# Optimization experiments

Hardware: AMD Instinct MI355X
Metric: run time of the kernel (lower is better)

Reference implementation:

```python
import jax, jax.numpy as jnp
import numpy as np

N_NODES = 50000
N_EDGES = 500000
H_DIM = 128
OUT_DIM = 16
N_RELS = 90
N_BASES = 4


def setup_inputs() -> dict:
    key = jax.random.key(0)
    ks = jax.random.split(key, 12)
    inp = {
        'node_ids': jnp.arange(N_NODES, dtype=jnp.int32),
        'src': jax.random.randint(ks[0], (N_EDGES,), 0, N_NODES, dtype=jnp.int32),
        'dst': jax.random.randint(ks[1], (N_EDGES,), 0, N_NODES, dtype=jnp.int32),
        'etype': jax.random.randint(ks[2], (N_EDGES,), 0, N_RELS, dtype=jnp.int32),
        'emb': jax.random.normal(ks[3], (N_NODES, H_DIM), jnp.float32),
        'basis1': jax.random.normal(ks[4], (N_BASES, H_DIM, H_DIM), jnp.float32) * (1.0 / np.sqrt(H_DIM)),
        'comp1': jax.random.normal(ks[5], (N_RELS, N_BASES), jnp.float32) * (1.0 / np.sqrt(N_BASES)),
        'loop_w1': jax.random.normal(ks[6], (H_DIM, H_DIM), jnp.float32) * (1.0 / np.sqrt(H_DIM)),
        'bias1': jnp.zeros((H_DIM,), jnp.float32),
        'basis2': jax.random.normal(ks[7], (N_BASES, H_DIM, OUT_DIM), jnp.float32) * (1.0 / np.sqrt(H_DIM)),
        'comp2': jax.random.normal(ks[8], (N_RELS, N_BASES), jnp.float32) * (1.0 / np.sqrt(N_BASES)),
        'loop_w2': jax.random.normal(ks[9], (H_DIM, OUT_DIM), jnp.float32) * (1.0 / np.sqrt(H_DIM)),
        'bias2': jnp.zeros((OUT_DIM,), jnp.float32),
    }
    return inp


def _rel_graph_conv(x, src, dst, etype, basis, comp, loop_w, bias, num_nodes):
    # Basis decomposition: W_r = sum_b comp[r,b] * basis[b].
    # Project node features through each basis first (N is smaller than E),
    # then combine per-edge with relation coefficients: avoids per-edge GEMM.
    xb = jnp.einsum('ni,bio->nbo', x, basis)            # [N, B, out]
    msg = jnp.einsum('eb,ebo->eo', comp[etype], xb[src])  # [E, out]
    agg = jax.ops.segment_sum(msg, dst, num_segments=num_nodes)  # [N, out]
    # apply_norm=True: divide aggregated messages by in-degree of dst.
    deg = jax.ops.segment_sum(jnp.ones((src.shape[0],), x.dtype), dst,
                              num_segments=num_nodes)
    h = agg * (1.0 / jnp.maximum(deg, 1.0))[:, None]
    # self_loop=True plus bias.
    return h + x @ loop_w + bias


def reference(node_ids, src, dst, etype, emb, basis1, comp1, loop_w1, bias1,
              basis2, comp2, loop_w2, bias2):
    n = emb.shape[0]
    x = emb[node_ids]                                   # embedding lookup
    h = jax.nn.relu(_rel_graph_conv(x, src, dst, etype, basis1, comp1,
                                    loop_w1, bias1, n))
    out = _rel_graph_conv(h, src, dst, etype, basis2, comp2, loop_w2, bias2, n)
    return out
```

## Files before the change

kernel.cpp:

```cpp
#include <hip/hip_runtime.h>
#include <hip/hip_bf16.h>

#define N_NODES 50000
#define N_EDGES 500000
#define H_DIM 128
#define OUT_DIM 16
#define KDIM 640

typedef short short8 __attribute__((ext_vector_type(8)));
typedef float f32x4 __attribute__((ext_vector_type(4)));
typedef float f32x2 __attribute__((ext_vector_type(2)));

__device__ inline unsigned short f2b(float f) {
  unsigned u = __float_as_uint(f);
  u += 0x7fffu + ((u >> 16) & 1u);
  return (unsigned short)(u >> 16);
}
__device__ inline float b2f(unsigned short u) {
  return __uint_as_float(((unsigned)u) << 16);
}

#define CONV_BLOCKS 6250
#define PREP_BLOCKS 360
#define INIT_BLOCKS 196
__global__ void prologue_kernel(const int* __restrict__ node_ids, const float* __restrict__ emb,
                                unsigned short* __restrict__ Abuf,
                                const float* __restrict__ basis1, const float* __restrict__ loop_w1,
                                const float* __restrict__ basis2, const float* __restrict__ loop_w2,
                                unsigned short* __restrict__ B1t, unsigned short* __restrict__ B2pt,
                                int* __restrict__ cntA, int* __restrict__ cntB,
                                int* __restrict__ counter) {
  int b = blockIdx.x;
  if (b < CONV_BLOCKS) {
    int tid = b * 256 + threadIdx.x;
    if (tid >= N_NODES * (H_DIM / 4)) return;
    int n = tid >> 5;
    int q = tid & 31;
    int id = node_ids[n];
    const float4 v = *reinterpret_cast<const float4*>(emb + (size_t)id * H_DIM + q * 4);
    uint2 p;
    p.x = (unsigned)f2b(v.x) | ((unsigned)f2b(v.y) << 16);
    p.y = (unsigned)f2b(v.z) | ((unsigned)f2b(v.w) << 16);
    *reinterpret_cast<uint2*>(Abuf + (size_t)n * KDIM + 512 + q * 4) = p;
  } else if (b < CONV_BLOCKS + PREP_BLOCKS) {
    int tid = (b - CONV_BLOCKS) * 256 + threadIdx.x;
    if (tid < 128 * KDIM) {
      int c = tid / KDIM, k = tid % KDIM;
      float v = (k < 512) ? basis1[k * 128 + c] : loop_w1[(k - 512) * 128 + c];
      B1t[c * KDIM + k] = f2b(v);
    } else if (tid < 128 * KDIM + 80 * 128) {
      int t2 = tid - 128 * KDIM;
      int c = t2 / 128, k = t2 % 128;
      float v = (c < 64) ? basis2[(c >> 4) * 128 * 16 + k * 16 + (c & 15)]
                         : loop_w2[k * 16 + (c - 64)];
      B2pt[c * 128 + k] = f2b(v);
    }
  } else {
    int i = (b - CONV_BLOCKS - PREP_BLOCKS) * 256 + threadIdx.x;
    if (i < N_NODES) {
      cntA[i] = 0;
      cntB[i] = 0;
    }
    if (i == 0) *counter = 0;
  }
}

__global__ void count_kernel(const int* __restrict__ dst, int* __restrict__ cnt) {
  for (int e = blockIdx.x * blockDim.x + threadIdx.x; e < N_EDGES; e += gridDim.x * blockDim.x)
    atomicAdd(&cnt[dst[e]], 1);
}

__global__ void alloc_kernel(const int* __restrict__ cnt, int* __restrict__ start,
                             int* __restrict__ counter) {
  int i = blockIdx.x * blockDim.x + threadIdx.x;
  int lane = threadIdx.x & 63;
  int c = (i < N_NODES) ? cnt[i] : 0;
  int incl = c;
#pragma unroll
  for (int off = 1; off < 64; off <<= 1) {
    int v = __shfl_up(incl, off, 64);
    if (lane >= off) incl += v;
  }
  int waveTotal = __shfl(incl, 63, 64);
  int base = 0;
  if (lane == 63) base = atomicAdd(counter, waveTotal);
  base = __shfl(base, 63, 64);
  if (i < N_NODES) start[i] = base + incl - c;
}

__global__ void fill_kernel(const int* __restrict__ src, const int* __restrict__ dst,
                            const int* __restrict__ et, const int* __restrict__ csr_start,
                            int* __restrict__ cnt, int2* __restrict__ csr_se) {
  for (int e = blockIdx.x * blockDim.x + threadIdx.x; e < N_EDGES; e += gridDim.x * blockDim.x) {
    int d = dst[e];
    int idx = csr_start[d] + atomicAdd(&cnt[d], 1);
    csr_se[idx] = make_int2(src[e], et[e]);
  }
}

__global__ __launch_bounds__(256) void agg_kernel(const int* __restrict__ csr_start,
                                                  const int* __restrict__ csr_cnt,
                                                  const int2* __restrict__ csr_se,
                                                  const float* __restrict__ comp,
                                                  unsigned short* __restrict__ Abuf) {
  int node = blockIdx.x * 4 + (threadIdx.x >> 6);
  if (node >= N_NODES) return;
  int lane = threadIdx.x & 63;
  int lo = __builtin_amdgcn_readfirstlane(csr_start[node]);
  int deg = __builtin_amdgcn_readfirstlane(csr_cnt[node]);
  int hi = lo + deg;

  f32x2 a0 = {0.f, 0.f}, a1 = {0.f, 0.f}, a2 = {0.f, 0.f}, a3 = {0.f, 0.f};
  const unsigned short* featb = Abuf + 512;
  const int laneoff = lane * 2;

#define EDGE_BODY(S, T)                                                              \
  {                                                                                  \
    unsigned u = *reinterpret_cast<const unsigned*>(featb + (size_t)(S)*KDIM + laneoff); \
    float4 c = *reinterpret_cast<const float4*>(comp + (T)*4);                       \
    f32x2 x;                                                                         \
    x.x = __uint_as_float(u << 16);                                                  \
    x.y = __uint_as_float(u & 0xffff0000u);                                          \
    a0 = __builtin_elementwise_fma((f32x2){c.x, c.x}, x, a0);                        \
    a1 = __builtin_elementwise_fma((f32x2){c.y, c.y}, x, a1);                        \
    a2 = __builtin_elementwise_fma((f32x2){c.z, c.z}, x, a2);                        \
    a3 = __builtin_elementwise_fma((f32x2){c.w, c.w}, x, a3);                        \
  }

  int e = lo;
  for (; e + 4 <= hi; e += 4) {
    int2 p0 = csr_se[e], p1 = csr_se[e + 1], p2 = csr_se[e + 2], p3 = csr_se[e + 3];
    int s0 = __builtin_amdgcn_readfirstlane(p0.x), t0 = __builtin_amdgcn_readfirstlane(p0.y);
    int s1 = __builtin_amdgcn_readfirstlane(p1.x), t1 = __builtin_amdgcn_readfirstlane(p1.y);
    int s2 = __builtin_amdgcn_readfirstlane(p2.x), t2 = __builtin_amdgcn_readfirstlane(p2.y);
    int s3 = __builtin_amdgcn_readfirstlane(p3.x), t3 = __builtin_amdgcn_readfirstlane(p3.y);
    EDGE_BODY(s0, t0)
    EDGE_BODY(s1, t1)
    EDGE_BODY(s2, t2)
    EDGE_BODY(s3, t3)
  }
  for (; e < hi; ++e) {
    int2 p = csr_se[e];
    int s0 = __builtin_amdgcn_readfirstlane(p.x), t0 = __builtin_amdgcn_readfirstlane(p.y);
    EDGE_BODY(s0, t0)
  }
#undef EDGE_BODY

  float inv = 1.0f / (float)(deg > 0 ? deg : 1);
  unsigned short* out = Abuf + (size_t)node * KDIM;
  unsigned p0w = (unsigned)f2b(a0.x * inv) | ((unsigned)f2b(a0.y * inv) << 16);
  unsigned p1w = (unsigned)f2b(a1.x * inv) | ((unsigned)f2b(a1.y * inv) << 16);
  unsigned p2w = (unsigned)f2b(a2.x * inv) | ((unsigned)f2b(a2.y * inv) << 16);
  unsigned p3w = (unsigned)f2b(a3.x * inv) | ((unsigned)f2b(a3.y * inv) << 16);
  *reinterpret_cast<unsigned*>(out + 0 * 128 + laneoff) = p0w;
  *reinterpret_cast<unsigned*>(out + 1 * 128 + laneoff) = p1w;
  *reinterpret_cast<unsigned*>(out + 2 * 128 + laneoff) = p2w;
  *reinterpret_cast<unsigned*>(out + 3 * 128 + laneoff) = p3w;
}

__global__ __launch_bounds__(256) void agg2_kernel(const int* __restrict__ csr_start,
                                                   const int* __restrict__ csr_cnt,
                                                   const int2* __restrict__ csr_se,
                                                   const float* __restrict__ comp,
                                                   const unsigned short* __restrict__ Abuf,
                                                   const float* __restrict__ bias2,
                                                   float* __restrict__ dout) {
  int node = blockIdx.x * 4 + (threadIdx.x >> 6);
  if (node >= N_NODES) return;
  int lane = threadIdx.x & 63;
  int bsel = lane >> 4;
  int o = lane & 15;
  int lo = __builtin_amdgcn_readfirstlane(csr_start[node]);
  int deg = __builtin_amdgcn_readfirstlane(csr_cnt[node]);
  int hi = lo + deg;

  float acc = 0.f;

#define EDGE2_BODY(S, T)                                                   \
  {                                                                        \
    unsigned short u = Abuf[(size_t)(S)*KDIM + lane];                      \
    float4 c = *reinterpret_cast<const float4*>(comp + (T)*4);             \
    float cb = (bsel < 2) ? ((bsel == 0) ? c.x : c.y)                      \
                          : ((bsel == 2) ? c.z : c.w);                     \
    acc = fmaf(cb, b2f(u), acc);                                           \
  }

  int e = lo;
  for (; e + 4 <= hi; e += 4) {
    int2 p0 = csr_se[e], p1 = csr_se[e + 1], p2 = csr_se[e + 2], p3 = csr_se[e + 3];
    int s0 = __builtin_amdgcn_readfirstlane(p0.x), t0 = __builtin_amdgcn_readfirstlane(p0.y);
    int s1 = __builtin_amdgcn_readfirstlane(p1.x), t1 = __builtin_amdgcn_readfirstlane(p1.y);
    int s2 = __builtin_amdgcn_readfirstlane(p2.x), t2 = __builtin_amdgcn_readfirstlane(p2.y);
    int s3 = __builtin_amdgcn_readfirstlane(p3.x), t3 = __builtin_amdgcn_readfirstlane(p3.y);
    EDGE2_BODY(s0, t0)
    EDGE2_BODY(s1, t1)
    EDGE2_BODY(s2, t2)
    EDGE2_BODY(s3, t3)
  }
  for (; e < hi; ++e) {
    int2 p = csr_se[e];
    int s0 = __builtin_amdgcn_readfirstlane(p.x), t0 = __builtin_amdgcn_readfirstlane(p.y);
    EDGE2_BODY(s0, t0)
  }
#undef EDGE2_BODY

  acc += __shfl_xor(acc, 16, 64);
  acc += __shfl_xor(acc, 32, 64);

  if (lane < 16) {
    float inv = 1.0f / (float)(deg > 0 ? deg : 1);
    float sl = b2f(Abuf[(size_t)node * KDIM + 64 + o]);
    dout[(size_t)node * OUT_DIM + o] = acc * inv + sl + bias2[o];
  }
}

template <int NC, int KT, bool RELU, bool HAS_BIAS>
__global__ __launch_bounds__(256) void gemm_kernel(const unsigned short* __restrict__ A,
                                                   int a_stride,
                                                   const unsigned short* __restrict__ Bt,
                                                   int bt_stride,
                                                   const float* __restrict__ bias,
                                                   unsigned short* __restrict__ outp,
                                                   int out_stride, int M) {
  __shared__ unsigned short As[64][64];
  __shared__ unsigned short Bs[NC][64];
  int wave = threadIdx.x >> 6;
  int lane = threadIdx.x & 63;
  int row0 = blockIdx.x * 64;
  f32x4 acc[NC / 16];
#pragma unroll
  for (int i = 0; i < NC / 16; ++i) acc[i] = (f32x4){0.f, 0.f, 0.f, 0.f};

  int ar = wave * 16 + (lane & 15);
  int kh = lane >> 4;

  for (int k0 = 0; k0 < KT; k0 += 64) {
#pragma unroll
    for (int p = 0; p < 2; ++p) {
      int cid = threadIdx.x + p * 256;
      int r = cid >> 3, c8 = cid & 7;
      int gr = row0 + r;
      short8 v = {};
      if (gr < M) v = *reinterpret_cast<const short8*>(A + (size_t)gr * a_stride + k0 + c8 * 8);
      *reinterpret_cast<short8*>(&As[r][(c8 ^ (r & 7)) * 8]) = v;
    }
    for (int cid = threadIdx.x; cid < NC * 8; cid += 256) {
      int r = cid >> 3, c8 = cid & 7;
      short8 v = *reinterpret_cast<const short8*>(Bt + (size_t)r * bt_stride + k0 + c8 * 8);
      *reinterpret_cast<short8*>(&Bs[r][(c8 ^ (r & 7)) * 8]) = v;
    }
    __syncthreads();
    short8 a0 = *reinterpret_cast<const short8*>(&As[ar][((kh) ^ (ar & 7)) * 8]);
    short8 a1 = *reinterpret_cast<const short8*>(&As[ar][((4 + kh) ^ (ar & 7)) * 8]);
#pragma unroll
    for (int ct = 0; ct < NC / 16; ++ct) {
      int bc = ct * 16 + (lane & 15);
      short8 b0 = *reinterpret_cast<const short8*>(&Bs[bc][((kh) ^ (bc & 7)) * 8]);
      short8 b1 = *reinterpret_cast<const short8*>(&Bs[bc][((4 + kh) ^ (bc & 7)) * 8]);
      acc[ct] = __builtin_amdgcn_mfma_f32_16x16x32_bf16(a0, b0, acc[ct], 0, 0, 0);
      acc[ct] = __builtin_amdgcn_mfma_f32_16x16x32_bf16(a1, b1, acc[ct], 0, 0, 0);
    }
    __syncthreads();
  }
  int col_l = lane & 15;
  int rb = row0 + wave * 16 + (lane >> 4) * 4;
#pragma unroll
  for (int ct = 0; ct < NC / 16; ++ct) {
    int col = ct * 16 + col_l;
    float bv = HAS_BIAS ? bias[col] : 0.f;
#pragma unroll
    for (int r = 0; r < 4; ++r) {
      int gr = rb + r;
      if (gr < M) {
        float v = acc[ct][r] + bv;
        if (RELU) v = fmaxf(v, 0.0f);
        outp[(size_t)gr * out_stride + col] = f2b(v);
      }
    }
  }
}

extern "C" void kernel_launch(void* const* d_in, const int* in_sizes, int n_in,
                              void* d_out, int out_size, void* d_ws, size_t ws_size,
                              hipStream_t stream) {
  const int* node_ids = (const int*)d_in[0];
  const int* src = (const int*)d_in[1];
  const int* dst = (const int*)d_in[2];
  const int* etype = (const int*)d_in[3];
  const float* emb = (const float*)d_in[4];
  const float* basis1 = (const float*)d_in[5];
  const float* comp1 = (const float*)d_in[6];
  const float* loop_w1 = (const float*)d_in[7];
  const float* bias1 = (const float*)d_in[8];
  const float* basis2 = (const float*)d_in[9];
  const float* comp2 = (const float*)d_in[10];
  const float* loop_w2 = (const float*)d_in[11];
  const float* bias2 = (const float*)d_in[12];
  (void)in_sizes; (void)n_in; (void)out_size; (void)ws_size;

  char* ws = (char*)d_ws;
  size_t off = 0;
  auto alloc = [&](size_t bytes) -> void* {
    void* p = ws + off;
    off += (bytes + 255) & ~(size_t)255;
    return p;
  };
  int* csr_start = (int*)alloc(N_NODES * sizeof(int));
  int* cntA = (int*)alloc(N_NODES * sizeof(int));
  int* cntB = (int*)alloc(N_NODES * sizeof(int));
  int* counter = (int*)alloc(sizeof(int));
  int2* csr_se = (int2*)alloc((size_t)N_EDGES * sizeof(int2));
  unsigned short* Abuf = (unsigned short*)alloc((size_t)N_NODES * KDIM * sizeof(unsigned short));
  unsigned short* B1t = (unsigned short*)alloc(128 * KDIM * sizeof(unsigned short));
  unsigned short* B2pt = (unsigned short*)alloc(80 * 128 * sizeof(unsigned short));

  prologue_kernel<<<CONV_BLOCKS + PREP_BLOCKS + INIT_BLOCKS, 256, 0, stream>>>(
      node_ids, emb, Abuf, basis1, loop_w1, basis2, loop_w2, B1t, B2pt, cntA, cntB, counter);
  count_kernel<<<1024, 256, 0, stream>>>(dst, cntA);
  alloc_kernel<<<(N_NODES + 255) / 256, 256, 0, stream>>>(cntA, csr_start, counter);
  fill_kernel<<<1024, 256, 0, stream>>>(src, dst, etype, csr_start, cntB, csr_se);

  agg_kernel<<<(N_NODES + 3) / 4, 256, 0, stream>>>(csr_start, cntA, csr_se, comp1, Abuf);
  gemm_kernel<128, KDIM, true, true><<<(N_NODES + 63) / 64, 256, 0, stream>>>(
      Abuf, KDIM, B1t, KDIM, bias1, Abuf + 512, KDIM, N_NODES);

  gemm_kernel<80, 128, false, false><<<(N_NODES + 63) / 64, 256, 0, stream>>>(
      Abuf + 512, KDIM, B2pt, 128, nullptr, Abuf, KDIM, N_NODES);
  agg2_kernel<<<(N_NODES + 3) / 4, 256, 0, stream>>>(csr_start, cntA, csr_se, comp2, Abuf,
                                                     bias2, (float*)d_out);
}
```

Measured before the change: 166.9 us.

## Batch CSR edge loads across lanes and add multi-row-tile GEMM blocking

The aggregation kernels now load up to 64 (src, etype) pairs at once, one per lane, and broadcast each with readlane. This replaces the serial per-edge scalar loads that sat on the dependency chain. The GEMM gains a BM template parameter, so the first-layer GEMM uses 128-row tiles with two row tiles per wave, reusing each B fragment across more MFMAs. The cost is higher register use and half as many blocks for the big GEMM, which may lower occupancy.

```diff
diff --git a/kernel.cpp b/kernel.cpp
--- a/kernel.cpp
+++ b/kernel.cpp
@@ -114,35 +114,33 @@
   const unsigned short* featb = Abuf + 512;
   const int laneoff = lane * 2;
 
-#define EDGE_BODY(S, T)                                                              \
-  {                                                                                  \
-    unsigned u = *reinterpret_cast<const unsigned*>(featb + (size_t)(S)*KDIM + laneoff); \
-    float4 c = *reinterpret_cast<const float4*>(comp + (T)*4);                       \
-    f32x2 x;                                                                         \
-    x.x = __uint_as_float(u << 16);                                                  \
-    x.y = __uint_as_float(u & 0xffff0000u);                                          \
-    a0 = __builtin_elementwise_fma((f32x2){c.x, c.x}, x, a0);                        \
-    a1 = __builtin_elementwise_fma((f32x2){c.y, c.y}, x, a1);                        \
-    a2 = __builtin_elementwise_fma((f32x2){c.z, c.z}, x, a2);                        \
-    a3 = __builtin_elementwise_fma((f32x2){c.w, c.w}, x, a3);                        \
-  }
-
-  int e = lo;
-  for (; e + 4 <= hi; e += 4) {
-    int2 p0 = csr_se[e], p1 = csr_se[e + 1], p2 = csr_se[e + 2], p3 = csr_se[e + 3];
-    int s0 = __builtin_amdgcn_readfirstlane(p0.x), t0 = __builtin_amdgcn_readfirstlane(p0.y);
-    int s1 = __builtin_amdgcn_readfirstlane(p1.x), t1 = __builtin_amdgcn_readfirstlane(p1.y);
-    int s2 = __builtin_amdgcn_readfirstlane(p2.x), t2 = __builtin_amdgcn_readfirstlane(p2.y);
-    int s3 = __builtin_amdgcn_readfirstlane(p3.x), t3 = __builtin_amdgcn_readfirstlane(p3.y);
-    EDGE_BODY(s0, t0)
-    EDGE_BODY(s1, t1)
-    EDGE_BODY(s2, t2)
-    EDGE_BODY(s3, t3)
-  }
-  for (; e < hi; ++e) {
-    int2 p = csr_se[e];
-    int s0 = __builtin_amdgcn_readfirstlane(p.x), t0 = __builtin_amdgcn_readfirstlane(p.y);
-    EDGE_BODY(s0, t0)
+#define EDGE_BODY(J)                                                                   \
+  {                                                                                    \
+    int s = __builtin_amdgcn_readlane(myse.x, (J));                                    \
+    int t = __builtin_amdgcn_readlane(myse.y, (J));                                    \
+    unsigned u = *reinterpret_cast<const unsigned*>(featb + s * KDIM + laneoff);       \
+    float4 c = *reinterpret_cast<const float4*>(comp + t * 4);                         \
+    f32x2 x;                                                                           \
+    x.x = __uint_as_float(u << 16);                                                    \
+    x.y = __uint_as_float(u & 0xffff0000u);                                            \
+    a0 = __builtin_elementwise_fma((f32x2){c.x, c.x}, x, a0);                          \
+    a1 = __builtin_elementwise_fma((f32x2){c.y, c.y}, x, a1);                          \
+    a2 = __builtin_elementwise_fma((f32x2){c.z, c.z}, x, a2);                          \
+    a3 = __builtin_elementwise_fma((f32x2){c.w, c.w}, x, a3);                          \
+  }
+
+  for (int e0 = lo; e0 < hi; e0 += 64) {
+    int nchunk = min(hi - e0, 64);
+    int2 myse = make_int2(0, 0);
+    if (e0 + lane < hi) myse = csr_se[e0 + lane];
+    int j = 0;
+    for (; j + 4 <= nchunk; j += 4) {
+      EDGE_BODY(j)
+      EDGE_BODY(j + 1)
+      EDGE_BODY(j + 2)
+      EDGE_BODY(j + 3)
+    }
+    for (; j < nchunk; ++j) { EDGE_BODY(j) }
   }
 #undef EDGE_BODY
 
@@ -176,31 +174,29 @@
 
   float acc = 0.f;
 
-#define EDGE2_BODY(S, T)                                                   \
+#define EDGE2_BODY(J)                                                      \
   {                                                                        \
-    unsigned short u = Abuf[(size_t)(S)*KDIM + lane];                      \
-    float4 c = *reinterpret_cast<const float4*>(comp + (T)*4);             \
+    int s = __builtin_amdgcn_readlane(myse.x, (J));                        \
+    int t = __builtin_amdgcn_readlane(myse.y, (J));                        \
+    unsigned short u = Abuf[s * KDIM + lane];                              \
+    float4 c = *reinterpret_cast<const float4*>(comp + t * 4);             \
     float cb = (bsel < 2) ? ((bsel == 0) ? c.x : c.y)                      \
                           : ((bsel == 2) ? c.z : c.w);                     \
     acc = fmaf(cb, b2f(u), acc);                                           \
   }
 
-  int e = lo;
-  for (; e + 4 <= hi; e += 4) {
-    int2 p0 = csr_se[e], p1 = csr_se[e + 1], p2 = csr_se[e + 2], p3 = csr_se[e + 3];
-    int s0 = __builtin_amdgcn_readfirstlane(p0.x), t0 = __builtin_amdgcn_readfirstlane(p0.y);
-    int s1 = __builtin_amdgcn_readfirstlane(p1.x), t1 = __builtin_amdgcn_readfirstlane(p1.y);
-    int s2 = __builtin_amdgcn_readfirstlane(p2.x), t2 = __builtin_amdgcn_readfirstlane(p2.y);
-    int s3 = __builtin_amdgcn_readfirstlane(p3.x), t3 = __builtin_amdgcn_readfirstlane(p3.y);
-    EDGE2_BODY(s0, t0)
-    EDGE2_BODY(s1, t1)
-    EDGE2_BODY(s2, t2)
-    EDGE2_BODY(s3, t3)
-  }
-  for (; e < hi; ++e) {
-    int2 p = csr_se[e];
-    int s0 = __builtin_amdgcn_readfirstlane(p.x), t0 = __builtin_amdgcn_readfirstlane(p.y);
-    EDGE2_BODY(s0, t0)
+  for (int e0 = lo; e0 < hi; e0 += 64) {
+    int nchunk = min(hi - e0, 64);
+    int2 myse = make_int2(0, 0);
+    if (e0 + lane < hi) myse = csr_se[e0 + lane];
+    int j = 0;
+    for (; j + 4 <= nchunk; j += 4) {
+      EDGE2_BODY(j)
+      EDGE2_BODY(j + 1)
+      EDGE2_BODY(j + 2)
+      EDGE2_BODY(j + 3)
+    }
+    for (; j < nchunk; ++j) { EDGE2_BODY(j) }
   }
 #undef EDGE2_BODY
 
@@ -214,7 +210,7 @@
   }
 }
 
-template <int NC, int KT, bool RELU, bool HAS_BIAS>
+template <int BM, int NC, int KT, bool RELU, bool HAS_BIAS>
 __global__ __launch_bounds__(256) void gemm_kernel(const unsigned short* __restrict__ A,
                                                    int a_stride,
                                                    const unsigned short* __restrict__ Bt,
@@ -222,21 +218,20 @@
                                                    const float* __restrict__ bias,
                                                    unsigned short* __restrict__ outp,
                                                    int out_stride, int M) {
-  __shared__ unsigned short As[64][64];
+  constexpr int RT = BM / 64;
+  __shared__ unsigned short As[BM][64];
   __shared__ unsigned short Bs[NC][64];
   int wave = threadIdx.x >> 6;
   int lane = threadIdx.x & 63;
-  int row0 = blockIdx.x * 64;
-  f32x4 acc[NC / 16];
-#pragma unroll
-  for (int i = 0; i < NC / 16; ++i) acc[i] = (f32x4){0.f, 0.f, 0.f, 0.f};
-
-  int ar = wave * 16 + (lane & 15);
+  int row0 = blockIdx.x * BM;
+  f32x4 acc[RT][NC / 16] = {};
+
   int kh = lane >> 4;
+  int cl = lane & 15;
 
   for (int k0 = 0; k0 < KT; k0 += 64) {
 #pragma unroll
-    for (int p = 0; p < 2; ++p) {
+    for (int p = 0; p < BM * 8 / 256; ++p) {
       int cid = threadIdx.x + p * 256;
       int r = cid >> 3, c8 = cid & 7;
       int gr = row0 + r;
@@ -250,31 +245,41 @@
       *reinterpret_cast<short8*>(&Bs[r][(c8 ^ (r & 7)) * 8]) = v;
     }
     __syncthreads();
-    short8 a0 = *reinterpret_cast<const short8*>(&As[ar][((kh) ^ (ar & 7)) * 8]);
-    short8 a1 = *reinterpret_cast<const short8*>(&As[ar][((4 + kh) ^ (ar & 7)) * 8]);
+    short8 af[RT][2];
+#pragma unroll
+    for (int rt = 0; rt < RT; ++rt) {
+      int ar = wave * (16 * RT) + rt * 16 + cl;
+      af[rt][0] = *reinterpret_cast<const short8*>(&As[ar][((kh) ^ (ar & 7)) * 8]);
+      af[rt][1] = *reinterpret_cast<const short8*>(&As[ar][((4 + kh) ^ (ar & 7)) * 8]);
+    }
 #pragma unroll
     for (int ct = 0; ct < NC / 16; ++ct) {
-      int bc = ct * 16 + (lane & 15);
+      int bc = ct * 16 + cl;
       short8 b0 = *reinterpret_cast<const short8*>(&Bs[bc][((kh) ^ (bc & 7)) * 8]);
       short8 b1 = *reinterpret_cast<const short8*>(&Bs[bc][((4 + kh) ^ (bc & 7)) * 8]);
-      acc[ct] = __builtin_amdgcn_mfma_f32_16x16x32_bf16(a0, b0, acc[ct], 0, 0, 0);
-      acc[ct] = __builtin_amdgcn_mfma_f32_16x16x32_bf16(a1, b1, acc[ct], 0, 0, 0);
+#pragma unroll
+      for (int rt = 0; rt < RT; ++rt) {
+        acc[rt][ct] = __builtin_amdgcn_mfma_f32_16x16x32_bf16(af[rt][0], b0, acc[rt][ct], 0, 0, 0);
+        acc[rt][ct] = __builtin_amdgcn_mfma_f32_16x16x32_bf16(af[rt][1], b1, acc[rt][ct], 0, 0, 0);
+      }
     }
     __syncthreads();
   }
-  int col_l = lane & 15;
-  int rb = row0 + wave * 16 + (lane >> 4) * 4;
-#pragma unroll
-  for (int ct = 0; ct < NC / 16; ++ct) {
-    int col = ct * 16 + col_l;
-    float bv = HAS_BIAS ? bias[col] : 0.f;
-#pragma unroll
-    for (int r = 0; r < 4; ++r) {
-      int gr = rb + r;
-      if (gr < M) {
-        float v = acc[ct][r] + bv;
-        if (RELU) v = fmaxf(v, 0.0f);
-        outp[(size_t)gr * out_stride + col] = f2b(v);
+#pragma unroll
+  for (int rt = 0; rt < RT; ++rt) {
+    int rb = row0 + wave * (16 * RT) + rt * 16 + (lane >> 4) * 4;
+#pragma unroll
+    for (int ct = 0; ct < NC / 16; ++ct) {
+      int col = ct * 16 + cl;
+      float bv = HAS_BIAS ? bias[col] : 0.f;
+#pragma unroll
+      for (int r = 0; r < 4; ++r) {
+        int gr = rb + r;
+        if (gr < M) {
+          float v = acc[rt][ct][r] + bv;
+          if (RELU) v = fmaxf(v, 0.0f);
+          outp[(size_t)gr * out_stride + col] = f2b(v);
+        }
       }
     }
   }
@@ -321,10 +326,10 @@
   fill_kernel<<<1024, 256, 0, stream>>>(src, dst, etype, csr_start, cntB, csr_se);
 
   agg_kernel<<<(N_NODES + 3) / 4, 256, 0, stream>>>(csr_start, cntA, csr_se, comp1, Abuf);
-  gemm_kernel<128, KDIM, true, true><<<(N_NODES + 63) / 64, 256, 0, stream>>>(
+  gemm_kernel<128, 128, KDIM, true, true><<<(N_NODES + 127) / 128, 256, 0, stream>>>(
       Abuf, KDIM, B1t, KDIM, bias1, Abuf + 512, KDIM, N_NODES);
 
-  gemm_kernel<80, 128, false, false><<<(N_NODES + 63) / 64, 256, 0, stream>>>(
+  gemm_kernel<64, 80, 128, false, false><<<(N_NODES + 63) / 64, 256, 0, stream>>>(
       Abuf + 512, KDIM, B2pt, 128, nullptr, Abuf, KDIM, N_NODES);
   agg2_kernel<<<(N_NODES + 3) / 4, 256, 0, stream>>>(csr_start, cntA, csr_se, comp2, Abuf,
                                                      bias2, (float*)d_out);
```

Measured after the change: 176.4 us. +5.7%, slower.
